# Optimization experiments

Measured on AMD Instinct MI355X. Metric: run time of the kernel, lower is better.

The kernel has to match this reference:

```python
import jax, jax.numpy as jnp
import numpy as np

E, T, K, H, I = 16, 512, 8, 2048, 1024  # experts, tokens, top-k, hidden, ffn half-width


def setup_inputs() -> dict:
    key = jax.random.key(0)
    ks = jax.random.split(key, 8)
    x = jax.random.normal(ks[0], (T, H), dtype=jnp.float32)
    expert_ids = jax.random.randint(ks[1], (T, K), 0, E, dtype=jnp.int32)
    # int8-valued weights stored as int32 (exactly representable)
    gmm1_weight = jax.random.randint(ks[2], (E, H, 2 * I), -127, 128, dtype=jnp.int32)
    gmm2_weight = jax.random.randint(ks[3], (E, I, H), -127, 128, dtype=jnp.int32)
    gmm1_weight_scale = jax.random.uniform(ks[4], (E, 2 * I), dtype=jnp.float32) * 1e-3
    gmm2_weight_scale = jax.random.uniform(ks[5], (E, H), dtype=jnp.float32) * 1e-3
    smooth_scales = jax.random.uniform(ks[6], (E, H), dtype=jnp.float32)
    expert_scales = jax.random.uniform(ks[7], (T, K), dtype=jnp.float32)
    return {"x": x, "expert_ids": expert_ids, "gmm1_weight": gmm1_weight,
            "gmm1_weight_scale": gmm1_weight_scale, "gmm2_weight": gmm2_weight,
            "gmm2_weight_scale": gmm2_weight_scale, "smooth_scales": smooth_scales,
            "expert_scales": expert_scales}


def _dynamic_quant(v):
    # per-token symmetric dynamic quant to int8 range (quant_mode=2 / quant_mode=1)
    s = jnp.max(jnp.abs(v), axis=-1, keepdims=True) / 127.0
    q = jnp.clip(jnp.round(v / s), -128.0, 127.0)  # kept in f32; values are exact small ints
    return q, s


def _grouped_mm(a, w, e_flat):
    # grouped GEMM: out[i] = a[i] @ w[e_flat[i]]. Disjoint expert masks -> masked full GEMMs summed.
    out = jnp.zeros((a.shape[0], w.shape[-1]), dtype=a.dtype)
    for e in range(w.shape[0]):
        mask = (e_flat == e)[:, None]
        out = out + jnp.where(mask, a, 0.0) @ w[e]
    return out


def reference(x, expert_ids, gmm1_weight, gmm1_weight_scale, gmm2_weight,
              gmm2_weight_scale, smooth_scales, expert_scales):
    # --- dispatch: per-token dynamic int8 quant + replicate each token K times ---
    xq, s0 = _dynamic_quant(x)                 # [T,H], [T,1]
    e_flat = expert_ids.reshape(-1)            # [T*K]
    xq_e = jnp.repeat(xq, K, axis=0)           # [T*K,H]
    s0_e = jnp.repeat(s0, K, axis=0)           # [T*K,1] == dynamic_scales / activation_scale
    w1 = gmm1_weight.astype(jnp.float32)       # int8 GEMM emulated exactly in f32
    w2 = gmm2_weight.astype(jnp.float32)
    # --- grouped GEMM 1 -> int32 accumulator values ---
    y1_i32 = _grouped_mm(xq_e, w1, e_flat)     # [T*K,2I]
    # --- fused dequant + SwiGLU (activate_left) + per-token dynamic requant ---
    y1f = y1_i32 * gmm1_weight_scale[e_flat] * s0_e
    act = jax.nn.silu(y1f[:, :I]) * y1f[:, I:]
    aq, s1 = _dynamic_quant(act)               # [T*K,I], [T*K,1]
    # --- grouped GEMM 2 + dequant (per-channel weight scale * per-token scale) ---
    y2_i32 = _grouped_mm(aq, w2, e_flat)       # [T*K,H]
    y2 = y2_i32 * gmm2_weight_scale[e_flat] * s1
    # --- combine: weighted sum over the K expert copies of each token ---
    out = jnp.einsum('tkh,tk->th', y2.reshape(T, K, H), expert_scales)
    return out
```

## Files before the change

### kernel.cpp

```cpp
#include <hip/hip_runtime.h>
#include <hip/hip_bf16.h>
#include <stdint.h>

#define E_   16
#define T_   512
#define KTOP 8
#define H_   2048
#define I_   1024
#define TK_  4096

typedef __attribute__((ext_vector_type(4))) int i32x4;

#define OFF_CNT     0
#define OFF_ROWMAX  4096
#define OFF_XQ      32768
#define OFF_S0      (OFF_XQ + T_*H_)
#define OFF_S1      (OFF_S0 + 4096)
#define OFF_LIST    (OFF_S1 + TK_*4)
#define OFF_ACT     (OFF_LIST + E_*TK_*4)
#define OFF_AQ      (OFF_ACT + (size_t)TK_*I_*4)
#define OFF_Y2      (OFF_AQ + (size_t)TK_*I_)

#define SCHEDB() __builtin_amdgcn_sched_barrier(0)

__global__ void k_zero(unsigned int* __restrict__ p) {
  int i = blockIdx.x * 256 + threadIdx.x;
  if (i < 5120) p[i] = 0;
}

__global__ void k_quant(const float* __restrict__ x, signed char* __restrict__ xq,
                        float* __restrict__ s0, const int* __restrict__ eids,
                        unsigned int* __restrict__ counts, int* __restrict__ row_list) {
  int t = blockIdx.x, tid = threadIdx.x;
  if (tid < KTOP) {
    int e = eids[t * KTOP + tid];
    int pos = (int)atomicAdd(&counts[e], 1u);
    row_list[e * TK_ + pos] = t * KTOP + tid;
  }
  const float4* xr = (const float4*)(x + (size_t)t * H_);
  float4 a = xr[tid * 2 + 0], b = xr[tid * 2 + 1];
  float m = fmaxf(
      fmaxf(fmaxf(fabsf(a.x), fabsf(a.y)), fmaxf(fabsf(a.z), fabsf(a.w))),
      fmaxf(fmaxf(fabsf(b.x), fabsf(b.y)), fmaxf(fabsf(b.z), fabsf(b.w))));
  for (int o = 32; o > 0; o >>= 1) m = fmaxf(m, __shfl_xor(m, o));
  __shared__ float wm[4];
  if ((tid & 63) == 0) wm[tid >> 6] = m;
  __syncthreads();
  m = fmaxf(fmaxf(wm[0], wm[1]), fmaxf(wm[2], wm[3]));
  float s = m / 127.0f;
  if (!(s > 0.f)) s = 1.0f;
  if (tid == 0) s0[t] = s;
  float v[8] = {a.x, a.y, a.z, a.w, b.x, b.y, b.z, b.w};
  unsigned int lo = 0, hi = 0;
#pragma unroll
  for (int j = 0; j < 4; ++j) {
    float qf = fminf(fmaxf(rintf(v[j] / s), -128.f), 127.f);
    lo |= ((unsigned)((int)qf & 0xFF)) << (8 * j);
  }
#pragma unroll
  for (int j = 0; j < 4; ++j) {
    float qf = fminf(fmaxf(rintf(v[4 + j] / s), -128.f), 127.f);
    hi |= ((unsigned)((int)qf & 0xFF)) << (8 * j);
  }
  ((uint2*)(xq + (size_t)t * H_))[tid] = make_uint2(lo, hi);
}

#define BM_   256
#define WSTR  2048

#define PACKU2(SRC) (make_uint2(                                          \
    ((SRC)[0] & 0xFF) | (((SRC)[1] & 0xFF) << 8) |                        \
    (((SRC)[2] & 0xFF) << 16) | ((SRC)[3] << 24),                         \
    ((SRC)[4] & 0xFF) | (((SRC)[5] & 0xFF) << 8) |                        \
    (((SRC)[6] & 0xFF) << 16) | ((SRC)[7] << 24)))

#define LOADB(BANK, TT)                                                   \
    _Pragma("unroll")                                                     \
    for (int j_ = 0; j_ < 8; ++j_)                                        \
      BANK[j_] = bsrc[(size_t)((TT) * 64 + brow0 + j_) * WSTR];

#define LOADA(BANK, TT)                                                   \
    _Pragma("unroll")                                                     \
    for (int mi_ = 0; mi_ < 2; ++mi_)                                     \
      BANK[mi_] = *(const i32x4*)(gA[mi_] + (TT) * 64);

#define WRITEB(BANK) do { *(uint2*)bdst = PACKU2(BANK); } while (0)

#define MFMAS(ABANK)                                                      \
    _Pragma("unroll")                                                     \
    for (int f_ = 0; f_ < 4; ++f_) {                                      \
      i32x4 bf_ = *(const i32x4*)(bsm + (f_ * 16 + l15) * 80 + l4 * 16);  \
      _Pragma("unroll")                                                   \
      for (int mi_ = 0; mi_ < 2; ++mi_)                                   \
        acc[mi_][f_] = __builtin_amdgcn_mfma_i32_16x16x64_i8(             \
            ABANK[mi_], bf_, acc[mi_][f_], 0, 0, 0);                      \
    }

#define TILE2(TT)                                                         \
    __syncthreads();                                                      \
    WRITEB(b0);                                                           \
    LOADB(b1, (TT) + 1); LOADA(a1, (TT) + 1); SCHEDB();                   \
    __syncthreads();                                                      \
    MFMAS(a0);                                                            \
    __syncthreads();                                                      \
    WRITEB(b1);                                                           \
    if ((TT) + 2 < NT) { LOADB(b0, (TT) + 2); LOADA(a0, (TT) + 2); }      \
    SCHEDB();                                                             \
    __syncthreads();                                                      \
    MFMAS(a1);

__launch_bounds__(512, 4)
__global__ void k_gemm1(const signed char* __restrict__ xq, const int* __restrict__ w1,
                        const float* __restrict__ ws1, const float* __restrict__ s0,
                        const unsigned int* __restrict__ counts,
                        const int* __restrict__ row_list,
                        float* __restrict__ act, unsigned int* __restrict__ rowmax) {
  __shared__ alignas(16) char bsm[64 * 80];
  int e = blockIdx.y;
  int cnt = (int)counts[e];
  if (cnt == 0) return;
  int p0 = blockIdx.x * 32;
  const int* rl = row_list + e * TK_;
  const int* we = w1 + (size_t)e * H_ * (2 * I_);
  const float* wsc = ws1 + (size_t)e * (2 * I_);

  int tid = threadIdx.x, w = tid >> 6, lane = tid & 63;
  int l15 = lane & 15, l4 = lane >> 4;

  int bcol = (lane < 32) ? (p0 + lane) : (I_ + p0 + (lane - 32));
  const int* bsrc = we + bcol;
  const int brow0 = w * 8;
  char* bdst = bsm + lane * 80 + w * 8;

  const int NT = H_ / 64;
  for (int ch = 0; ch * BM_ < cnt; ++ch) {
    int rbase = ch * BM_;
    const signed char* gA[2];
#pragma unroll
    for (int mi = 0; mi < 2; ++mi) {
      int gr = rbase + w * 32 + mi * 16 + l15;
      int tok = rl[gr < cnt ? gr : 0] >> 3;
      gA[mi] = xq + (size_t)tok * H_ + l4 * 16;
    }
    i32x4 acc[2][4];
#pragma unroll
    for (int i = 0; i < 2; ++i)
#pragma unroll
      for (int n = 0; n < 4; ++n) acc[i][n] = (i32x4)(0);

    int b0[8], b1[8];
    i32x4 a0[2], a1[2];
    LOADB(b0, 0); LOADA(a0, 0); SCHEDB();
    for (int t = 0; t < NT; t += 2) { TILE2(t); }

#pragma unroll
    for (int mi = 0; mi < 2; ++mi) {
#pragma unroll
      for (int r = 0; r < 4; ++r) {
        int gr = rbase + w * 32 + mi * 16 + l4 * 4 + r;
        bool valid = gr < cnt;
        int irow = rl[valid ? gr : 0];
        float s0v = s0[irow >> 3];
        float rowm = 0.f, av0 = 0.f, av1 = 0.f;
#pragma unroll
        for (int n = 0; n < 2; ++n) {
          int colL = p0 + n * 16 + l15;
          float yl = (float)acc[mi][n][r] * wsc[colL] * s0v;
          float yr = (float)acc[mi][n + 2][r] * wsc[I_ + colL] * s0v;
          float actv = (yl / (1.f + expf(-yl))) * yr;
          if (n == 0) av0 = actv; else av1 = actv;
          rowm = fmaxf(rowm, fabsf(actv));
        }
        rowm = fmaxf(rowm, __shfl_xor(rowm, 1));
        rowm = fmaxf(rowm, __shfl_xor(rowm, 2));
        rowm = fmaxf(rowm, __shfl_xor(rowm, 4));
        rowm = fmaxf(rowm, __shfl_xor(rowm, 8));
        if (valid) {
          act[(size_t)irow * I_ + p0 + l15] = av0;
          act[(size_t)irow * I_ + p0 + 16 + l15] = av1;
          if (l15 == 0) atomicMax(rowmax + irow, __float_as_uint(rowm));
        }
      }
    }
  }
}

__global__ void k_requant(const float* __restrict__ act, const unsigned int* __restrict__ rowmax,
                          signed char* __restrict__ aq, float* __restrict__ s1) {
  int i = blockIdx.x, tid = threadIdx.x;
  float m = __uint_as_float(rowmax[i]);
  float s = (m > 0.f) ? (m / 127.0f) : 1.0f;
  if (tid == 0) s1[i] = s;
  float4 v = ((const float4*)(act + (size_t)i * I_))[tid];
  float vv[4] = {v.x, v.y, v.z, v.w};
  unsigned int pk = 0;
#pragma unroll
  for (int j = 0; j < 4; ++j) {
    float qf = fminf(fmaxf(rintf(vv[j] / s), -128.f), 127.f);
    pk |= ((unsigned)((int)qf & 0xFF)) << (8 * j);
  }
  ((unsigned int*)(aq + (size_t)i * I_))[tid] = pk;
}

__launch_bounds__(512, 4)
__global__ void k_gemm2(const signed char* __restrict__ aq, const int* __restrict__ w2,
                        const float* __restrict__ ws2, const float* __restrict__ s1,
                        const float* __restrict__ es,
                        const unsigned int* __restrict__ counts,
                        const int* __restrict__ row_list,
                        __hip_bfloat16* __restrict__ y2h) {
  __shared__ alignas(16) char bsm[64 * 80];
  int e = blockIdx.y;
  int cnt = (int)counts[e];
  if (cnt == 0) return;
  int n0 = blockIdx.x * 64;
  const int* rl = row_list + e * TK_;
  const int* we = w2 + (size_t)e * I_ * H_;
  const float* wsc = ws2 + (size_t)e * H_;

  int tid = threadIdx.x, w = tid >> 6, lane = tid & 63;
  int l15 = lane & 15, l4 = lane >> 4;

  const int* bsrc = we + n0 + lane;
  const int brow0 = w * 8;
  char* bdst = bsm + lane * 80 + w * 8;

  const int NT = I_ / 64;
  for (int ch = 0; ch * BM_ < cnt; ++ch) {
    int rbase = ch * BM_;
    const signed char* gA[2];
#pragma unroll
    for (int mi = 0; mi < 2; ++mi) {
      int gr = rbase + w * 32 + mi * 16 + l15;
      gA[mi] = aq + (size_t)rl[gr < cnt ? gr : 0] * I_ + l4 * 16;
    }
    i32x4 acc[2][4];
#pragma unroll
    for (int i = 0; i < 2; ++i)
#pragma unroll
      for (int n = 0; n < 4; ++n) acc[i][n] = (i32x4)(0);

    int b0[8], b1[8];
    i32x4 a0[2], a1[2];
    LOADB(b0, 0); LOADA(a0, 0); SCHEDB();
    for (int t = 0; t < NT; t += 2) { TILE2(t); }

#pragma unroll
    for (int mi = 0; mi < 2; ++mi) {
#pragma unroll
      for (int r = 0; r < 4; ++r) {
        int gr = rbase + w * 32 + mi * 16 + l4 * 4 + r;
        if (gr < cnt) {
          int irow = rl[gr];
          float sc = s1[irow] * es[irow];
#pragma unroll
          for (int n = 0; n < 4; ++n) {
            int c = n0 + n * 16 + l15;
            float v = (float)acc[mi][n][r] * wsc[c] * sc;
            y2h[(size_t)irow * H_ + c] = __float2bfloat16(v);
          }
        }
      }
    }
  }
}

__global__ void k_combine(const __hip_bfloat16* __restrict__ y2h, float* __restrict__ out) {
  int idx = blockIdx.x * 256 + threadIdx.x;
  int t = idx >> 8;
  int h0 = (idx & 255) * 8;
  float s[8];
#pragma unroll
  for (int j = 0; j < 8; ++j) s[j] = 0.f;
#pragma unroll
  for (int k = 0; k < KTOP; ++k) {
    const __hip_bfloat16* p = y2h + ((size_t)(t * KTOP + k) * H_ + h0);
    uint4 u = *(const uint4*)p;
    const __hip_bfloat16* b = (const __hip_bfloat16*)&u;
#pragma unroll
    for (int j = 0; j < 8; ++j) s[j] += __bfloat162float(b[j]);
  }
  float4 o0 = make_float4(s[0], s[1], s[2], s[3]);
  float4 o1 = make_float4(s[4], s[5], s[6], s[7]);
  float4* dst = (float4*)(out + (size_t)t * H_ + h0);
  dst[0] = o0; dst[1] = o1;
}

extern "C" void kernel_launch(void* const* d_in, const int* in_sizes, int n_in,
                              void* d_out, int out_size, void* d_ws, size_t ws_size,
                              hipStream_t stream) {
  const float* x   = (const float*)d_in[0];
  const int*   eid = (const int*)d_in[1];
  const int*   w1  = (const int*)d_in[2];
  const float* ws1 = (const float*)d_in[3];
  const int*   w2  = (const int*)d_in[4];
  const float* ws2 = (const float*)d_in[5];
  const float* es  = (const float*)d_in[7];
  float* out = (float*)d_out;
  char* ws = (char*)d_ws;

  unsigned int*  counts   = (unsigned int*)(ws + OFF_CNT);
  unsigned int*  rowmax   = (unsigned int*)(ws + OFF_ROWMAX);
  signed char*   xq       = (signed char*)(ws + OFF_XQ);
  float*         s0       = (float*)(ws + OFF_S0);
  float*         s1       = (float*)(ws + OFF_S1);
  int*           row_list = (int*)(ws + OFF_LIST);
  float*         act      = (float*)(ws + OFF_ACT);
  signed char*   aq       = (signed char*)(ws + OFF_AQ);
  __hip_bfloat16* y2h     = (__hip_bfloat16*)(ws + OFF_Y2);

  k_zero<<<20, 256, 0, stream>>>((unsigned int*)ws);
  k_quant<<<T_, 256, 0, stream>>>(x, xq, s0, eid, counts, row_list);
  k_gemm1<<<dim3(32, E_), 512, 0, stream>>>(xq, w1, ws1, s0, counts, row_list, act, rowmax);
  k_requant<<<TK_, 256, 0, stream>>>(act, rowmax, aq, s1);
  k_gemm2<<<dim3(32, E_), 512, 0, stream>>>(aq, w2, ws2, s1, es, counts, row_list, y2h);
  k_combine<<<(T_ * H_ / 8) / 256, 256, 0, stream>>>(y2h, out);
}
```

Baseline: 202.2 us.

## Double-buffer LDS B tiles with triple register prefetch and 384-row chunks

Replaces the two-tile ping-pong with a software pipeline in both grouped GEMMs: B tiles are double-buffered in LDS, prefetched three tiles ahead in registers, and A fragments are prefetched two ahead. The four barriers per two tiles become one lgkmcnt wait plus barrier per tile. Each wave now covers 48 rows (three MFMA row groups) instead of 32, so a chunk holds 384 rows and each B tile is reused more. The cost is higher register pressure under launch_bounds(512,4), which risks spills, and more padded rows per chunk for experts whose row count is not a multiple of 384.

```diff
diff --git a/kernel.cpp b/kernel.cpp
--- a/kernel.cpp
+++ b/kernel.cpp
@@ -21,7 +21,10 @@
 #define OFF_AQ      (OFF_ACT + (size_t)TK_*I_*4)
 #define OFF_Y2      (OFF_AQ + (size_t)TK_*I_)
 
-#define SCHEDB() __builtin_amdgcn_sched_barrier(0)
+#define LBAR() do {                                             \
+    asm volatile("s_waitcnt lgkmcnt(0)" ::: "memory");          \
+    __builtin_amdgcn_s_barrier();                               \
+  } while (0)
 
 __global__ void k_zero(unsigned int* __restrict__ p) {
   int i = blockIdx.x * 256 + threadIdx.x;
@@ -65,8 +68,9 @@
   ((uint2*)(xq + (size_t)t * H_))[tid] = make_uint2(lo, hi);
 }
 
-#define BM_   256
-#define WSTR  2048
+#define BM_    384
+#define WSTR   2048
+#define BSTR   5120
 
 #define PACKU2(SRC) (make_uint2(                                          \
     ((SRC)[0] & 0xFF) | (((SRC)[1] & 0xFF) << 8) |                        \
@@ -81,33 +85,44 @@
 
 #define LOADA(BANK, TT)                                                   \
     _Pragma("unroll")                                                     \
-    for (int mi_ = 0; mi_ < 2; ++mi_)                                     \
+    for (int mi_ = 0; mi_ < 3; ++mi_)                                     \
       BANK[mi_] = *(const i32x4*)(gA[mi_] + (TT) * 64);
 
-#define WRITEB(BANK) do { *(uint2*)bdst = PACKU2(BANK); } while (0)
-
-#define MFMAS(ABANK)                                                      \
+#define WRITEB(BANK, BUF)                                                 \
+    *(uint2*)(bsm + (BUF) * BSTR + lane * 80 + w * 8) = PACKU2(BANK);
+
+#define MFMAS(BUF, ABANK)                                                 \
     _Pragma("unroll")                                                     \
     for (int f_ = 0; f_ < 4; ++f_) {                                      \
-      i32x4 bf_ = *(const i32x4*)(bsm + (f_ * 16 + l15) * 80 + l4 * 16);  \
+      i32x4 bf_ = *(const i32x4*)(bsm + (BUF) * BSTR +                    \
+                                  (f_ * 16 + l15) * 80 + l4 * 16);        \
       _Pragma("unroll")                                                   \
-      for (int mi_ = 0; mi_ < 2; ++mi_)                                   \
+      for (int mi_ = 0; mi_ < 3; ++mi_)                                   \
         acc[mi_][f_] = __builtin_amdgcn_mfma_i32_16x16x64_i8(             \
-            ABANK[mi_], bf_, acc[mi_][f_], 0, 0, 0);                      \
-    }
-
-#define TILE2(TT)                                                         \
-    __syncthreads();                                                      \
-    WRITEB(b0);                                                           \
-    LOADB(b1, (TT) + 1); LOADA(a1, (TT) + 1); SCHEDB();                   \
-    __syncthreads();                                                      \
-    MFMAS(a0);                                                            \
-    __syncthreads();                                                      \
-    WRITEB(b1);                                                           \
-    if ((TT) + 2 < NT) { LOADB(b0, (TT) + 2); LOADA(a0, (TT) + 2); }      \
-    SCHEDB();                                                             \
-    __syncthreads();                                                      \
-    MFMAS(a1);
+            ABANK, bf_, acc[mi_][f_], 0, 0, 0);                           \
+    }
+
+#define KSWEEP(NT)                                                        \
+    LOADB(bB[0], 0); LOADA(aA0, 0);                                       \
+    LOADB(bB[1], 1); LOADA(aA1, 1);                                       \
+    LOADB(bB[2], 2);                                                      \
+    WRITEB(bB[0], 0);                                                     \
+    LBAR();                                                               \
+    _Pragma("unroll")                                                     \
+    for (int t = 0; t < (NT); ++t) {                                      \
+      if ((t & 1) == 0) {                                                 \
+        MFMAS(0, aA0[mi_]);                                               \
+      } else {                                                            \
+        MFMAS(1, aA1[mi_]);                                               \
+      }                                                                   \
+      if (t + 1 < (NT)) { WRITEB(bB[(t + 1) % 3], (t + 1) & 1); }         \
+      if (t + 2 < (NT)) {                                                 \
+        if ((t & 1) == 0) { LOADA(aA0, t + 2); }                          \
+        else              { LOADA(aA1, t + 2); }                          \
+      }                                                                   \
+      if (t + 3 < (NT)) { LOADB(bB[t % 3], t + 3); }                      \
+      LBAR();                                                             \
+    }
 
 __launch_bounds__(512, 4)
 __global__ void k_gemm1(const signed char* __restrict__ xq, const int* __restrict__ w1,
@@ -115,7 +130,7 @@
                         const unsigned int* __restrict__ counts,
                         const int* __restrict__ row_list,
                         float* __restrict__ act, unsigned int* __restrict__ rowmax) {
-  __shared__ alignas(16) char bsm[64 * 80];
+  __shared__ alignas(16) char bsm[2 * BSTR];
   int e = blockIdx.y;
   int cnt = (int)counts[e];
   if (cnt == 0) return;
@@ -130,34 +145,32 @@
   int bcol = (lane < 32) ? (p0 + lane) : (I_ + p0 + (lane - 32));
   const int* bsrc = we + bcol;
   const int brow0 = w * 8;
-  char* bdst = bsm + lane * 80 + w * 8;
 
   const int NT = H_ / 64;
   for (int ch = 0; ch * BM_ < cnt; ++ch) {
     int rbase = ch * BM_;
-    const signed char* gA[2];
-#pragma unroll
-    for (int mi = 0; mi < 2; ++mi) {
-      int gr = rbase + w * 32 + mi * 16 + l15;
+    const signed char* gA[3];
+#pragma unroll
+    for (int mi = 0; mi < 3; ++mi) {
+      int gr = rbase + w * 48 + mi * 16 + l15;
       int tok = rl[gr < cnt ? gr : 0] >> 3;
       gA[mi] = xq + (size_t)tok * H_ + l4 * 16;
     }
-    i32x4 acc[2][4];
-#pragma unroll
-    for (int i = 0; i < 2; ++i)
+    i32x4 acc[3][4];
+#pragma unroll
+    for (int i = 0; i < 3; ++i)
 #pragma unroll
       for (int n = 0; n < 4; ++n) acc[i][n] = (i32x4)(0);
 
-    int b0[8], b1[8];
-    i32x4 a0[2], a1[2];
-    LOADB(b0, 0); LOADA(a0, 0); SCHEDB();
-    for (int t = 0; t < NT; t += 2) { TILE2(t); }
-
-#pragma unroll
-    for (int mi = 0; mi < 2; ++mi) {
+    int bB[3][8];
+    i32x4 aA0[3], aA1[3];
+    KSWEEP(NT);
+
+#pragma unroll
+    for (int mi = 0; mi < 3; ++mi) {
 #pragma unroll
       for (int r = 0; r < 4; ++r) {
-        int gr = rbase + w * 32 + mi * 16 + l4 * 4 + r;
+        int gr = rbase + w * 48 + mi * 16 + l4 * 4 + r;
         bool valid = gr < cnt;
         int irow = rl[valid ? gr : 0];
         float s0v = s0[irow >> 3];
@@ -209,7 +222,7 @@
                         const unsigned int* __restrict__ counts,
                         const int* __restrict__ row_list,
                         __hip_bfloat16* __restrict__ y2h) {
-  __shared__ alignas(16) char bsm[64 * 80];
+  __shared__ alignas(16) char bsm[2 * BSTR];
   int e = blockIdx.y;
   int cnt = (int)counts[e];
   if (cnt == 0) return;
@@ -223,33 +236,31 @@
 
   const int* bsrc = we + n0 + lane;
   const int brow0 = w * 8;
-  char* bdst = bsm + lane * 80 + w * 8;
 
   const int NT = I_ / 64;
   for (int ch = 0; ch * BM_ < cnt; ++ch) {
     int rbase = ch * BM_;
-    const signed char* gA[2];
-#pragma unroll
-    for (int mi = 0; mi < 2; ++mi) {
-      int gr = rbase + w * 32 + mi * 16 + l15;
+    const signed char* gA[3];
+#pragma unroll
+    for (int mi = 0; mi < 3; ++mi) {
+      int gr = rbase + w * 48 + mi * 16 + l15;
       gA[mi] = aq + (size_t)rl[gr < cnt ? gr : 0] * I_ + l4 * 16;
     }
-    i32x4 acc[2][4];
-#pragma unroll
-    for (int i = 0; i < 2; ++i)
+    i32x4 acc[3][4];
+#pragma unroll
+    for (int i = 0; i < 3; ++i)
 #pragma unroll
       for (int n = 0; n < 4; ++n) acc[i][n] = (i32x4)(0);
 
-    int b0[8], b1[8];
-    i32x4 a0[2], a1[2];
-    LOADB(b0, 0); LOADA(a0, 0); SCHEDB();
-    for (int t = 0; t < NT; t += 2) { TILE2(t); }
-
-#pragma unroll
-    for (int mi = 0; mi < 2; ++mi) {
+    int bB[3][8];
+    i32x4 aA0[3], aA1[3];
+    KSWEEP(NT);
+
+#pragma unroll
+    for (int mi = 0; mi < 3; ++mi) {
 #pragma unroll
       for (int r = 0; r < 4; ++r) {
-        int gr = rbase + w * 32 + mi * 16 + l4 * 4 + r;
+        int gr = rbase + w * 48 + mi * 16 + l4 * 4 + r;
         if (gr < cnt) {
           int irow = rl[gr];
           float sc = s1[irow] * es[irow];
```

Result: slower. 513.6 us (+154.0%).
